# Performance work log

Hardware: AMD Instinct MI355X
Metric: run time of the kernel (lower is better)

Reference implementation:

```python
import jax, jax.numpy as jnp
import numpy as np
from jax import lax

# LiteMSA config: in_ch=256, out_ch=256, dim=8, heads=32, total_dim=256, scales=(3,)
DIM = 8
QKV_CH = 768          # 3 * total_dim
PW_GROUPS = 96        # 3 * heads


def setup_inputs() -> dict:
    key = jax.random.key(0)
    ks = jax.random.split(key, 5)
    x = jax.random.normal(ks[0], (16, 256, 64, 64), jnp.float32)
    w_qkv = jax.random.normal(ks[1], (768, 256), jnp.float32) * 0.02      # 1x1 conv
    w_dw = jax.random.normal(ks[2], (768, 1, 3, 3), jnp.float32) * 0.02   # depthwise 3x3
    w_pw = jax.random.normal(ks[3], (768, 8, 1, 1), jnp.float32) * 0.02   # grouped 1x1, 96 groups
    w_proj = jax.random.normal(ks[4], (256, 512), jnp.float32) * 0.02     # 1x1 conv
    bn_gamma = jnp.ones((256,), jnp.float32)
    bn_beta = jnp.zeros((256,), jnp.float32)
    bn_mean = jnp.zeros((256,), jnp.float32)
    bn_var = jnp.ones((256,), jnp.float32)
    return {"x": x, "w_qkv": w_qkv, "w_dw": w_dw, "w_pw": w_pw, "w_proj": w_proj,
            "bn_gamma": bn_gamma, "bn_beta": bn_beta, "bn_mean": bn_mean, "bn_var": bn_var}


def reference(x, w_qkv, w_dw, w_pw, w_proj, bn_gamma, bn_beta, bn_mean, bn_var):
    B, _, H, W = x.shape
    dn = ("NCHW", "OIHW", "NCHW")
    # qkv 1x1 conv
    qkv = jnp.einsum("bchw,oc->bohw", x, w_qkv)  # [B,768,H,W]
    # multi-scale aggregation: depthwise 3x3 -> grouped 1x1
    agg = lax.conv_general_dilated(qkv, w_dw, (1, 1), "SAME",
                                   dimension_numbers=dn, feature_group_count=QKV_CH)
    agg = lax.conv_general_dilated(agg, w_pw, (1, 1), "SAME",
                                   dimension_numbers=dn, feature_group_count=PW_GROUPS)
    ms = jnp.concatenate([qkv, agg], axis=1)  # [B,1536,H,W]
    # [B, heads_total=64, N=H*W, 3*dim]
    ms = ms.reshape(B, -1, 3 * DIM, H * W).transpose(0, 1, 3, 2)
    q = jax.nn.relu(ms[..., :DIM])
    k = jax.nn.relu(ms[..., DIM:2 * DIM])
    v = ms[..., 2 * DIM:]
    # pad v with ones for normalizer channel
    v = jnp.concatenate([v, jnp.ones(v.shape[:-1] + (1,), v.dtype)], axis=-1)  # [B,h,N,dim+1]
    kv = jnp.einsum("bhnd,bhne->bhde", k, v)   # [B,h,dim,dim+1]
    out = jnp.einsum("bhnd,bhde->bhne", q, kv)  # [B,h,N,dim+1]
    out = out[..., :DIM] / (out[..., DIM:] + 1e-15)
    out = out.transpose(0, 1, 3, 2).reshape(B, -1, H, W)  # [B,512,H,W]
    # proj 1x1 conv + BatchNorm (inference, running stats)
    y = jnp.einsum("bchw,oc->bohw", out, w_proj)
    inv = bn_gamma / jnp.sqrt(bn_var + 1e-5)
    y = y * inv[None, :, None, None] + (bn_beta - bn_mean * inv)[None, :, None, None]
    return y
```

## Files before the change

kernel.cpp:

```cpp
#include <hip/hip_runtime.h>
#include <hip/hip_bf16.h>


#define NB 16
#define CQKV 768
#define P4096 4096

typedef __bf16 bf16x8 __attribute__((ext_vector_type(8)));
typedef float f32x4 __attribute__((ext_vector_type(4)));

__device__ __forceinline__ ushort f2bf(float f) {
    union { float f; unsigned int u; } x; x.f = f;
    unsigned int u = x.u;
    unsigned int r = (u + 0x7FFFu + ((u >> 16) & 1u)) >> 16;
    return (ushort)r;
}
__device__ __forceinline__ float bf2f(ushort u) {
    union { unsigned int u; float f; } x; x.u = ((unsigned int)u) << 16;
    return x.f;
}
__device__ __forceinline__ unsigned int pk2bf(float x, float y) {
    __hip_bfloat162 h = __float22bfloat162_rn(make_float2(x, y));
    union { __hip_bfloat162 b; unsigned int u; } c; c.b = h; return c.u;
}
__device__ __forceinline__ void stage_hi8(const float* v, ushort* dh) {
    union { unsigned int u[4]; uint4 q; } H;
    #pragma unroll
    for (int i = 0; i < 4; i++) H.u[i] = pk2bf(v[2 * i], v[2 * i + 1]);
    *(uint4*)dh = H.q;
}
__device__ __forceinline__ void stage_hilo8(const float* v, ushort* dh, ushort* dl) {
    union { unsigned int u[4]; uint4 q; } H, L;
    #pragma unroll
    for (int i = 0; i < 4; i++) {
        unsigned int h = pk2bf(v[2 * i], v[2 * i + 1]);
        H.u[i] = h;
        float f0 = __uint_as_float(h << 16);
        float f1 = __uint_as_float(h & 0xffff0000u);
        L.u[i] = pk2bf(v[2 * i] - f0, v[2 * i + 1] - f1);
    }
    *(uint4*)dh = H.q;
    *(uint4*)dl = L.q;
}

__global__ __launch_bounds__(256) void gemm_qkv_q(
    const float* __restrict__ A,
    const float* __restrict__ X,
    ushort* __restrict__ Cbf,
    float*  __restrict__ qplane)
{
    const int n0 = blockIdx.x * 64;
    const int m0 = blockIdx.y * 64;
    const int b  = blockIdx.z;
    const int t  = threadIdx.x;
    const int wave = t >> 6, lane = t & 63, quad = lane >> 4, l15 = lane & 15;

    __shared__ __align__(16) ushort AsH[64][40];
    __shared__ __align__(16) ushort AsL[64][40];
    __shared__ __align__(16) ushort BsH[64][40];
    __shared__ __align__(16) ushort BsL[64][40];

    f32x4 acc[4];
    #pragma unroll
    for (int nt = 0; nt < 4; nt++)
        #pragma unroll
        for (int r = 0; r < 4; r++) acc[nt][r] = 0.0f;

    const int am = t >> 2, ak = (t & 3) * 8;
    const int arow_v = m0 + am;
    const int arow_p = (arow_v >> 3) * 24 + (arow_v & 7);
    const int bn = t & 63, kg = (t >> 6) * 8;

    for (int k0 = 0; k0 < 256; k0 += 32) {
        float av[8];
        *(float4*)&av[0] = *(const float4*)(A + (size_t)arow_p * 256 + k0 + ak);
        *(float4*)&av[4] = *(const float4*)(A + (size_t)arow_p * 256 + k0 + ak + 4);
        float bv[8];
        #pragma unroll
        for (int i = 0; i < 8; i++)
            bv[i] = X[((size_t)b * 256 + k0 + kg + i) * P4096 + n0 + bn];

        __syncthreads();
        stage_hilo8(av, &AsH[am][ak], &AsL[am][ak]);
        stage_hilo8(bv, &BsH[bn][kg], &BsL[bn][kg]);
        __syncthreads();

        bf16x8 afh = *(const bf16x8*)&AsH[wave * 16 + l15][quad * 8];
        bf16x8 afl = *(const bf16x8*)&AsL[wave * 16 + l15][quad * 8];
        #pragma unroll
        for (int nt = 0; nt < 4; nt++) {
            bf16x8 bfh = *(const bf16x8*)&BsH[nt * 16 + l15][quad * 8];
            bf16x8 bfl = *(const bf16x8*)&BsL[nt * 16 + l15][quad * 8];
            acc[nt] = __builtin_amdgcn_mfma_f32_16x16x32_bf16(afh, bfh, acc[nt], 0, 0, 0);
            acc[nt] = __builtin_amdgcn_mfma_f32_16x16x32_bf16(afl, bfh, acc[nt], 0, 0, 0);
            acc[nt] = __builtin_amdgcn_mfma_f32_16x16x32_bf16(afh, bfl, acc[nt], 0, 0, 0);
        }
    }

    #pragma unroll
    for (int nt = 0; nt < 4; nt++) {
        #pragma unroll
        for (int r = 0; r < 4; r++) {
            int rv = m0 + wave * 16 + quad * 4 + r;
            int rp = (rv >> 3) * 24 + (rv & 7);
            int col = n0 + nt * 16 + l15;
            float v = acc[nt][r];
            Cbf[((size_t)b * CQKV + rp) * P4096 + col] = f2bf(v);
            qplane[((size_t)b * 256 + rv) * P4096 + col] = v;
        }
    }
}

__global__ __launch_bounds__(256) void gemm_qkv_kv(
    const float* __restrict__ A, const float* __restrict__ X,
    ushort* __restrict__ Cbf)
{
    const int n0 = blockIdx.x * 64;
    const int m0 = blockIdx.y * 64;
    const int b  = blockIdx.z;
    const int t  = threadIdx.x;
    const int wave = t >> 6, lane = t & 63, quad = lane >> 4, l15 = lane & 15;

    __shared__ __align__(16) ushort As[64][40];
    __shared__ __align__(16) ushort Bs[64][40];

    f32x4 acc[4];
    #pragma unroll
    for (int nt = 0; nt < 4; nt++)
        #pragma unroll
        for (int r = 0; r < 4; r++) acc[nt][r] = 0.0f;

    const int am = t >> 2, ak = (t & 3) * 8;
    const int arow_v = m0 + am;
    const int arow_p = (arow_v >> 4) * 24 + 8 + (arow_v & 15);
    const int bn = t & 63, kg = (t >> 6) * 8;

    for (int k0 = 0; k0 < 256; k0 += 32) {
        float av[8];
        *(float4*)&av[0] = *(const float4*)(A + (size_t)arow_p * 256 + k0 + ak);
        *(float4*)&av[4] = *(const float4*)(A + (size_t)arow_p * 256 + k0 + ak + 4);
        float bv[8];
        #pragma unroll
        for (int i = 0; i < 8; i++)
            bv[i] = X[((size_t)b * 256 + k0 + kg + i) * P4096 + n0 + bn];

        __syncthreads();
        stage_hi8(av, &As[am][ak]);
        stage_hi8(bv, &Bs[bn][kg]);
        __syncthreads();

        bf16x8 af = *(const bf16x8*)&As[wave * 16 + l15][quad * 8];
        #pragma unroll
        for (int nt = 0; nt < 4; nt++) {
            bf16x8 bf = *(const bf16x8*)&Bs[nt * 16 + l15][quad * 8];
            acc[nt] = __builtin_amdgcn_mfma_f32_16x16x32_bf16(af, bf, acc[nt], 0, 0, 0);
        }
    }

    #pragma unroll
    for (int nt = 0; nt < 4; nt++) {
        #pragma unroll
        for (int r = 0; r < 4; r++) {
            int rv = m0 + wave * 16 + quad * 4 + r;
            int rp = (rv >> 4) * 24 + 8 + (rv & 15);
            int col = n0 + nt * 16 + l15;
            Cbf[((size_t)b * CQKV + rp) * P4096 + col] = f2bf(acc[nt][r]);
        }
    }
}

__global__ __launch_bounds__(256) void qfix_kernel(
    float* __restrict__ qplane, const float* __restrict__ w_qkv,
    const float* __restrict__ x)
{
    size_t i = (size_t)blockIdx.x * 256 + threadIdx.x;
    float q = qplane[i];
    if (fabsf(q) >= 1e-4f) return;
    int p   = (int)(i & 4095);
    int qch = (int)((i >> 12) & 255);
    int b   = (int)(i >> 20);
    int row = (qch >> 3) * 24 + (qch & 7);
    const float* wr = w_qkv + (size_t)row * 256;
    const float* xr = x + (size_t)b * 256 * P4096 + p;
    double s = 0.0;
    for (int c = 0; c < 256; c++)
        s += (double)wr[c] * (double)xr[(size_t)c * P4096];
    qplane[i] = (float)s;
}

__global__ __launch_bounds__(512, 8) void dwpw_kernel(
    const ushort* __restrict__ qkv, const float* __restrict__ wdw,
    const float* __restrict__ wpw, ushort* __restrict__ agg)
{
    const int rt = blockIdx.x;
    const int g  = blockIdx.y;
    const int b  = blockIdx.z;
    const int t  = threadIdx.x;
    const int r0 = rt * 16;
    const int cg = g * 8;

    __shared__ __align__(16) ushort tile[8][18][80];

    const ushort* src = qkv + ((size_t)(b * CQKV + cg)) * P4096;

    if (t < 288) {
        int ch = t / 36;
        int rr = (t % 36) >> 1;
        int side = t & 1;
        *(uint4*)&tile[ch][rr][side * 72] = make_uint4(0, 0, 0, 0);
    }
    #pragma unroll
    for (int i = 0; i < 3; i++) {
        int id = t + i * 512;
        if (id < 1152) {
            int ch  = id / 144;
            int rem = id - ch * 144;
            int rr  = rem >> 3;
            int oct = (rem & 7) * 8;
            int grow = r0 - 1 + rr;
            uint4 v = make_uint4(0, 0, 0, 0);
            if (grow >= 0 && grow < 64)
                v = *(const uint4*)(src + (size_t)ch * P4096 + (size_t)grow * 64 + oct);
            *(uint4*)&tile[ch][rr][8 + oct] = v;
        }
    }
    __syncthreads();

    const int kc  = t & 31;
    const int row = t >> 5;
    const float* wdwg = wdw + (size_t)cg * 9;
    const float* wpwg = wpw + (size_t)cg * 8;

    float acc0[8], acc1[8];
    #pragma unroll
    for (int oi = 0; oi < 8; oi++) { acc0[oi] = 0.0f; acc1[oi] = 0.0f; }

    #pragma unroll
    for (int c = 0; c < 8; c++) {
        float dv0 = 0.0f, dv1 = 0.0f;
        #pragma unroll
        for (int dy = 0; dy < 3; dy++) {
            const ushort* rp = &tile[c][row + dy][2 * kc + 4];
            unsigned int u1 = *(const unsigned int*)(rp + 2);
            unsigned int u2 = *(const unsigned int*)(rp + 4);
            unsigned int u3 = *(const unsigned int*)(rp + 6);
            float xm1 = __uint_as_float(u1 & 0xffff0000u);
            float x0  = __uint_as_float(u2 << 16);
            float x1  = __uint_as_float(u2 & 0xffff0000u);
            float x2  = __uint_as_float(u3 << 16);
            float w0 = wdwg[c * 9 + dy * 3 + 0];
            float w1 = wdwg[c * 9 + dy * 3 + 1];
            float w2 = wdwg[c * 9 + dy * 3 + 2];
            dv0 = fmaf(w0, xm1, dv0); dv0 = fmaf(w1, x0, dv0); dv0 = fmaf(w2, x1, dv0);
            dv1 = fmaf(w0, x0,  dv1); dv1 = fmaf(w1, x1, dv1); dv1 = fmaf(w2, x2, dv1);
        }
        #pragma unroll
        for (int oi = 0; oi < 8; oi++) {
            float w = wpwg[oi * 8 + c];
            acc0[oi] = fmaf(w, dv0, acc0[oi]);
            acc1[oi] = fmaf(w, dv1, acc1[oi]);
        }
    }

    size_t obase = ((size_t)(b * CQKV + cg)) * P4096 + (size_t)(r0 + row) * 64 + 2 * kc;
    #pragma unroll
    for (int oi = 0; oi < 8; oi++) {
        unsigned int u = (unsigned int)f2bf(acc0[oi]) |
                         ((unsigned int)f2bf(acc1[oi]) << 16);
        *(unsigned int*)&agg[obase + (size_t)oi * P4096] = u;
    }
}

__global__ __launch_bounds__(256) void kv_kernel(
    const ushort* __restrict__ qkv, const ushort* __restrict__ agg,
    float* __restrict__ kv)
{
    const int h = blockIdx.x, b = blockIdx.y, t = threadIdx.x;
    const ushort* src = (h < 32)
        ? qkv + ((size_t)(b * CQKV + h * 24)) * P4096
        : agg + ((size_t)(b * CQKV + (h - 32) * 24)) * P4096;

    float acc[72];
    #pragma unroll
    for (int i = 0; i < 72; i++) acc[i] = 0.0f;

    for (int pi = 0; pi < 16; pi++) {
        int p = t + pi * 256;
        float kvv[8], vv[8];
        #pragma unroll
        for (int d = 0; d < 8; d++) {
            float xk = bf2f(src[(size_t)(8 + d) * P4096 + p]);
            kvv[d] = xk > 0.0f ? xk : 0.0f;
        }
        #pragma unroll
        for (int e = 0; e < 8; e++) vv[e] = bf2f(src[(size_t)(16 + e) * P4096 + p]);
        #pragma unroll
        for (int d = 0; d < 8; d++) {
            #pragma unroll
            for (int e = 0; e < 8; e++) acc[d * 9 + e] += kvv[d] * vv[e];
            acc[d * 9 + 8] += kvv[d];
        }
    }

    #pragma unroll
    for (int i = 0; i < 72; i++) {
        float v = acc[i];
        #pragma unroll
        for (int off = 32; off > 0; off >>= 1) v += __shfl_xor(v, off, 64);
        acc[i] = v;
    }
    __shared__ float part[4][72];
    int wave = t >> 6, lane = t & 63;
    if (lane == 0) {
        #pragma unroll
        for (int i = 0; i < 72; i++) part[wave][i] = acc[i];
    }
    __syncthreads();
    if (t < 72)
        kv[((size_t)b * 64 + h) * 72 + t] = part[0][t] + part[1][t] + part[2][t] + part[3][t];
}

__global__ __launch_bounds__(256) void attn_out_kernel(
    const float* __restrict__ qplane, ushort* __restrict__ agg,
    const float* __restrict__ kv)
{
    const int pt = blockIdx.x, h = blockIdx.y, b = blockIdx.z, t = threadIdx.x;
    __shared__ float kvs[72];
    if (t < 72) kvs[t] = kv[((size_t)b * 64 + h) * 72 + t];
    __syncthreads();

    const bool lohead = (h < 32);
    const float* srcf = lohead
        ? qplane + ((size_t)(b * 256 + h * 8)) * P4096 : nullptr;
    const ushort* srcb = lohead ? nullptr
        : agg + ((size_t)(b * CQKV + (h - 32) * 24)) * P4096;

    int p = pt * 256 + t;
    float num[8]; float den = 0.0f;
    #pragma unroll
    for (int e = 0; e < 8; e++) num[e] = 0.0f;
    #pragma unroll
    for (int d = 0; d < 8; d++) {
        float q = lohead ? srcf[(size_t)d * P4096 + p]
                         : bf2f(srcb[(size_t)d * P4096 + p]);
        q = q > 0.0f ? q : 0.0f;
        #pragma unroll
        for (int e = 0; e < 8; e++) num[e] += q * kvs[d * 9 + e];
        den += q * kvs[d * 9 + 8];
    }
    float rd = 1.0f / (den + 1e-15f);
    ushort* dst = agg + ((size_t)(b * CQKV + (h / 2) * 24 + 8 + (h % 2) * 8)) * P4096 + p;
    #pragma unroll
    for (int e = 0; e < 8; e++)
        dst[(size_t)e * P4096] = f2bf(num[e] * rd);
}

__global__ __launch_bounds__(256) void gemm_proj(
    const float* __restrict__ A,
    const ushort* __restrict__ Bagg,
    float* __restrict__ Y,
    const float* __restrict__ bn_g, const float* __restrict__ bn_b,
    const float* __restrict__ bn_m, const float* __restrict__ bn_v)
{
    const int n0 = blockIdx.x * 64;
    const int m0 = blockIdx.y * 64;
    const int b  = blockIdx.z;
    const int t  = threadIdx.x;
    const int wave = t >> 6, lane = t & 63, quad = lane >> 4, l15 = lane & 15;

    __shared__ __align__(16) ushort As[64][40];
    __shared__ __align__(16) ushort Bs[64][40];

    f32x4 acc[4];
    #pragma unroll
    for (int nt = 0; nt < 4; nt++)
        #pragma unroll
        for (int r = 0; r < 4; r++) acc[nt][r] = 0.0f;

    const int am = t >> 2, ak = (t & 3) * 8;
    const int bn = t & 63, kg = (t >> 6) * 8;

    for (int k0 = 0; k0 < 512; k0 += 32) {
        float av[8];
        *(float4*)&av[0] = *(const float4*)(A + (size_t)(m0 + am) * 512 + k0 + ak);
        *(float4*)&av[4] = *(const float4*)(A + (size_t)(m0 + am) * 512 + k0 + ak + 4);
        ushort bu[8];
        #pragma unroll
        for (int i = 0; i < 8; i++) {
            int kk = k0 + kg + i;
            int amch = (kk >> 4) * 24 + 8 + (kk & 15);
            bu[i] = Bagg[((size_t)b * CQKV + amch) * P4096 + n0 + bn];
        }

        __syncthreads();
        stage_hi8(av, &As[am][ak]);
        {
            union { ushort us[8]; uint4 q; } Bp;
            #pragma unroll
            for (int i = 0; i < 8; i++) Bp.us[i] = bu[i];
            *(uint4*)&Bs[bn][kg] = Bp.q;
        }
        __syncthreads();

        bf16x8 af = *(const bf16x8*)&As[wave * 16 + l15][quad * 8];
        #pragma unroll
        for (int nt = 0; nt < 4; nt++) {
            bf16x8 bf = *(const bf16x8*)&Bs[nt * 16 + l15][quad * 8];
            acc[nt] = __builtin_amdgcn_mfma_f32_16x16x32_bf16(af, bf, acc[nt], 0, 0, 0);
        }
    }

    #pragma unroll
    for (int nt = 0; nt < 4; nt++) {
        #pragma unroll
        for (int r = 0; r < 4; r++) {
            int row = m0 + wave * 16 + quad * 4 + r;
            int col = n0 + nt * 16 + l15;
            float inv = bn_g[row] / sqrtf(bn_v[row] + 1e-5f);
            float v = acc[nt][r] * inv + (bn_b[row] - bn_m[row] * inv);
            Y[((size_t)b * 256 + row) * P4096 + col] = v;
        }
    }
}

extern "C" void kernel_launch(void* const* d_in, const int* in_sizes, int n_in,
                              void* d_out, int out_size, void* d_ws, size_t ws_size,
                              hipStream_t stream) {
    const float* x      = (const float*)d_in[0];
    const float* w_qkv  = (const float*)d_in[1];
    const float* w_dw   = (const float*)d_in[2];
    const float* w_pw   = (const float*)d_in[3];
    const float* w_proj = (const float*)d_in[4];
    const float* bn_g   = (const float*)d_in[5];
    const float* bn_b   = (const float*)d_in[6];
    const float* bn_m   = (const float*)d_in[7];
    const float* bn_v   = (const float*)d_in[8];
    float* y = (float*)d_out;

    char* ws = (char*)d_ws;
    ushort* qkv_bf = (ushort*)(ws);
    float*  qplane = (float*) (ws + 100663296);
    ushort* agg_bf = (ushort*)(ws + 167772160);
    float*  kvbuf  = (float*)d_out;

    gemm_qkv_q<<<dim3(64, 4, NB), 256, 0, stream>>>(w_qkv, x, qkv_bf, qplane);
    gemm_qkv_kv<<<dim3(64, 8, NB), 256, 0, stream>>>(w_qkv, x, qkv_bf);

    qfix_kernel<<<65536, 256, 0, stream>>>(qplane, w_qkv, x);

    dwpw_kernel<<<dim3(4, 96, NB), 512, 0, stream>>>(qkv_bf, w_dw, w_pw, agg_bf);

    kv_kernel<<<dim3(64, NB), 256, 0, stream>>>(qkv_bf, agg_bf, kvbuf);

    attn_out_kernel<<<dim3(16, 64, NB), 256, 0, stream>>>(qplane, agg_bf, kvbuf);

    gemm_proj<<<dim3(64, 4, NB), 256, 0, stream>>>(
        w_proj, agg_bf, y, bn_g, bn_b, bn_m, bn_v);
}
```

Measured before the change: 457.1 us.

## Pre-convert inputs to swizzled bf16 and fuse QKV GEMMs with LDS direct loads

```diff
diff --git a/kernel.cpp b/kernel.cpp
--- a/kernel.cpp
+++ b/kernel.cpp
@@ -8,6 +8,8 @@
 
 typedef __bf16 bf16x8 __attribute__((ext_vector_type(8)));
 typedef float f32x4 __attribute__((ext_vector_type(4)));
+
+#define MFMA_BF16 __builtin_amdgcn_mfma_f32_16x16x32_bf16
 
 __device__ __forceinline__ ushort f2bf(float f) {
     union { float f; unsigned int u; } x; x.f = f;
@@ -29,143 +31,204 @@
     for (int i = 0; i < 4; i++) H.u[i] = pk2bf(v[2 * i], v[2 * i + 1]);
     *(uint4*)dh = H.q;
 }
-__device__ __forceinline__ void stage_hilo8(const float* v, ushort* dh, ushort* dl) {
-    union { unsigned int u[4]; uint4 q; } H, L;
-    #pragma unroll
-    for (int i = 0; i < 4; i++) {
-        unsigned int h = pk2bf(v[2 * i], v[2 * i + 1]);
-        H.u[i] = h;
-        float f0 = __uint_as_float(h << 16);
-        float f1 = __uint_as_float(h & 0xffff0000u);
-        L.u[i] = pk2bf(v[2 * i] - f0, v[2 * i + 1] - f1);
-    }
-    *(uint4*)dh = H.q;
-    *(uint4*)dl = L.q;
-}
-
-__global__ __launch_bounds__(256) void gemm_qkv_q(
-    const float* __restrict__ A,
-    const float* __restrict__ X,
-    ushort* __restrict__ Cbf,
-    float*  __restrict__ qplane)
-{
-    const int n0 = blockIdx.x * 64;
-    const int m0 = blockIdx.y * 64;
+
+__device__ __forceinline__ void gload16(void* lds, const void* g) {
+    __builtin_amdgcn_global_load_lds(
+        (const __attribute__((address_space(1))) void*)g,
+        (__attribute__((address_space(3))) void*)lds, 16, 0, 0);
+}
+
+__global__ __launch_bounds__(128) void conv_w(
+    const float* __restrict__ W, ushort* __restrict__ Ah, ushort* __restrict__ Al)
+{
+    const int rv = blockIdx.x;
+    const int t  = threadIdx.x;
+    int phys;
+    if (rv < 256) phys = (rv >> 3) * 24 + (rv & 7);
+    else { int r2 = rv - 256; phys = (r2 >> 4) * 24 + 8 + (r2 & 15); }
+    int c = t * 2;
+    float w0 = W[(size_t)phys * 256 + c];
+    float w1 = W[(size_t)phys * 256 + c + 1];
+    unsigned int h = pk2bf(w0, w1);
+    float f0 = __uint_as_float(h << 16);
+    float f1 = __uint_as_float(h & 0xffff0000u);
+    unsigned int l = pk2bf(w0 - f0, w1 - f1);
+    int sl = ((c >> 3) & 3) ^ ((rv >> 1) & 3);
+    int idx = (c & ~31) + sl * 8 + (c & 7);
+    *(unsigned int*)&Ah[(size_t)rv * 256 + idx] = h;
+    *(unsigned int*)&Al[(size_t)rv * 256 + idx] = l;
+}
+
+__global__ __launch_bounds__(256) void conv_x(
+    const float* __restrict__ X, ushort* __restrict__ XTh, ushort* __restrict__ XTl)
+{
+    const int pt = blockIdx.x;
+    const int ct = blockIdx.y;
+    const int b  = blockIdx.z;
+    const int t  = threadIdx.x;
+    const int p0 = pt * 64, c0 = ct * 64;
+
+    __shared__ float tile[64][65];
+
+    {
+        int cr = t >> 2, pc = (t & 3) * 16;
+        const float* xr = X + ((size_t)b * 256 + c0 + cr) * P4096 + p0 + pc;
+        float4 v0 = *(const float4*)xr;
+        float4 v1 = *(const float4*)(xr + 4);
+        float4 v2 = *(const float4*)(xr + 8);
+        float4 v3 = *(const float4*)(xr + 12);
+        float* d = &tile[cr][pc];
+        d[0]=v0.x; d[1]=v0.y; d[2]=v0.z; d[3]=v0.w;
+        d[4]=v1.x; d[5]=v1.y; d[6]=v1.z; d[7]=v1.w;
+        d[8]=v2.x; d[9]=v2.y; d[10]=v2.z; d[11]=v2.w;
+        d[12]=v3.x; d[13]=v3.y; d[14]=v3.z; d[15]=v3.w;
+    }
+    __syncthreads();
+
+    #pragma unroll
+    for (int pass = 0; pass < 2; pass++) {
+        int tp = t >> 2;
+        int cc = (t & 3) + pass * 4;
+        int p  = p0 + tp;
+        float v[8];
+        #pragma unroll
+        for (int j = 0; j < 8; j++) v[j] = tile[cc * 8 + j][tp];
+        union { unsigned int u[4]; uint4 q; } H, L;
+        #pragma unroll
+        for (int i = 0; i < 4; i++) {
+            unsigned int h = pk2bf(v[2 * i], v[2 * i + 1]);
+            H.u[i] = h;
+            float f0 = __uint_as_float(h << 16);
+            float f1 = __uint_as_float(h & 0xffff0000u);
+            L.u[i] = pk2bf(v[2 * i] - f0, v[2 * i + 1] - f1);
+        }
+        int c = c0 + cc * 8;
+        int sl = ((c >> 3) & 3) ^ ((p >> 1) & 3);
+        size_t idx = ((size_t)b * P4096 + p) * 256 + (c & ~31) + sl * 8;
+        *(uint4*)&XTh[idx] = H.q;
+        *(uint4*)&XTl[idx] = L.q;
+    }
+}
+
+__global__ __launch_bounds__(256, 3) void gemm_fused(
+    const ushort* __restrict__ Ah, const ushort* __restrict__ Al,
+    const ushort* __restrict__ Bh, const ushort* __restrict__ Bl,
+    ushort* __restrict__ Cbf, float* __restrict__ qplane)
+{
+    const int mt = blockIdx.x;
+    const int n0 = blockIdx.y * 128;
     const int b  = blockIdx.z;
     const int t  = threadIdx.x;
     const int wave = t >> 6, lane = t & 63, quad = lane >> 4, l15 = lane & 15;
-
-    __shared__ __align__(16) ushort AsH[64][40];
-    __shared__ __align__(16) ushort AsL[64][40];
-    __shared__ __align__(16) ushort BsH[64][40];
-    __shared__ __align__(16) ushort BsL[64][40];
-
-    f32x4 acc[4];
-    #pragma unroll
-    for (int nt = 0; nt < 4; nt++)
-        #pragma unroll
-        for (int r = 0; r < 4; r++) acc[nt][r] = 0.0f;
-
-    const int am = t >> 2, ak = (t & 3) * 8;
-    const int arow_v = m0 + am;
-    const int arow_p = (arow_v >> 3) * 24 + (arow_v & 7);
-    const int bn = t & 63, kg = (t >> 6) * 8;
-
-    for (int k0 = 0; k0 < 256; k0 += 32) {
-        float av[8];
-        *(float4*)&av[0] = *(const float4*)(A + (size_t)arow_p * 256 + k0 + ak);
-        *(float4*)&av[4] = *(const float4*)(A + (size_t)arow_p * 256 + k0 + ak + 4);
-        float bv[8];
-        #pragma unroll
-        for (int i = 0; i < 8; i++)
-            bv[i] = X[((size_t)b * 256 + k0 + kg + i) * P4096 + n0 + bn];
-
-        __syncthreads();
-        stage_hilo8(av, &AsH[am][ak], &AsL[am][ak]);
-        stage_hilo8(bv, &BsH[bn][kg], &BsL[bn][kg]);
-        __syncthreads();
-
-        bf16x8 afh = *(const bf16x8*)&AsH[wave * 16 + l15][quad * 8];
-        bf16x8 afl = *(const bf16x8*)&AsL[wave * 16 + l15][quad * 8];
-        #pragma unroll
-        for (int nt = 0; nt < 4; nt++) {
-            bf16x8 bfh = *(const bf16x8*)&BsH[nt * 16 + l15][quad * 8];
-            bf16x8 bfl = *(const bf16x8*)&BsL[nt * 16 + l15][quad * 8];
-            acc[nt] = __builtin_amdgcn_mfma_f32_16x16x32_bf16(afh, bfh, acc[nt], 0, 0, 0);
-            acc[nt] = __builtin_amdgcn_mfma_f32_16x16x32_bf16(afl, bfh, acc[nt], 0, 0, 0);
-            acc[nt] = __builtin_amdgcn_mfma_f32_16x16x32_bf16(afh, bfl, acc[nt], 0, 0, 0);
-        }
-    }
-
-    #pragma unroll
-    for (int nt = 0; nt < 4; nt++) {
-        #pragma unroll
-        for (int r = 0; r < 4; r++) {
-            int rv = m0 + wave * 16 + quad * 4 + r;
-            int rp = (rv >> 3) * 24 + (rv & 7);
-            int col = n0 + nt * 16 + l15;
-            float v = acc[nt][r];
-            Cbf[((size_t)b * CQKV + rp) * P4096 + col] = f2bf(v);
-            qplane[((size_t)b * 256 + rv) * P4096 + col] = v;
-        }
-    }
-}
-
-__global__ __launch_bounds__(256) void gemm_qkv_kv(
-    const float* __restrict__ A, const float* __restrict__ X,
-    ushort* __restrict__ Cbf)
-{
-    const int n0 = blockIdx.x * 64;
-    const int m0 = blockIdx.y * 64;
-    const int b  = blockIdx.z;
-    const int t  = threadIdx.x;
-    const int wave = t >> 6, lane = t & 63, quad = lane >> 4, l15 = lane & 15;
-
-    __shared__ __align__(16) ushort As[64][40];
-    __shared__ __align__(16) ushort Bs[64][40];
-
-    f32x4 acc[4];
-    #pragma unroll
-    for (int nt = 0; nt < 4; nt++)
-        #pragma unroll
-        for (int r = 0; r < 4; r++) acc[nt][r] = 0.0f;
-
-    const int am = t >> 2, ak = (t & 3) * 8;
-    const int arow_v = m0 + am;
-    const int arow_p = (arow_v >> 4) * 24 + 8 + (arow_v & 15);
-    const int bn = t & 63, kg = (t >> 6) * 8;
-
-    for (int k0 = 0; k0 < 256; k0 += 32) {
-        float av[8];
-        *(float4*)&av[0] = *(const float4*)(A + (size_t)arow_p * 256 + k0 + ak);
-        *(float4*)&av[4] = *(const float4*)(A + (size_t)arow_p * 256 + k0 + ak + 4);
-        float bv[8];
-        #pragma unroll
-        for (int i = 0; i < 8; i++)
-            bv[i] = X[((size_t)b * 256 + k0 + kg + i) * P4096 + n0 + bn];
-
-        __syncthreads();
-        stage_hi8(av, &As[am][ak]);
-        stage_hi8(bv, &Bs[bn][kg]);
-        __syncthreads();
-
-        bf16x8 af = *(const bf16x8*)&As[wave * 16 + l15][quad * 8];
-        #pragma unroll
-        for (int nt = 0; nt < 4; nt++) {
-            bf16x8 bf = *(const bf16x8*)&Bs[nt * 16 + l15][quad * 8];
-            acc[nt] = __builtin_amdgcn_mfma_f32_16x16x32_bf16(af, bf, acc[nt], 0, 0, 0);
-        }
-    }
-
-    #pragma unroll
-    for (int nt = 0; nt < 4; nt++) {
-        #pragma unroll
-        for (int r = 0; r < 4; r++) {
-            int rv = m0 + wave * 16 + quad * 4 + r;
-            int rp = (rv >> 4) * 24 + 8 + (rv & 15);
-            int col = n0 + nt * 16 + l15;
-            Cbf[((size_t)b * CQKV + rp) * P4096 + col] = f2bf(acc[nt][r]);
-        }
+    const int wr = wave >> 1, wc = wave & 1;
+    const int M0 = mt * 128;
+
+    __shared__ __align__(16) ushort AsH[128 * 32];
+    __shared__ __align__(16) ushort AsL[128 * 32];
+    __shared__ __align__(16) ushort BsH[128 * 32];
+    __shared__ __align__(16) ushort BsL[128 * 32];
+
+    int aoff[4], boff[4];
+    #pragma unroll
+    for (int i = 0; i < 4; i++) {
+        int ra = wr * 64 + i * 16 + l15;
+        aoff[i] = ra * 64 + ((quad ^ ((ra >> 1) & 3)) << 4);
+        int rb = wc * 64 + i * 16 + l15;
+        boff[i] = rb * 64 + ((quad ^ ((rb >> 1) & 3)) << 4);
+    }
+
+    const int srow = t >> 2;
+    const int schunk = (t & 3) * 8;
+    const size_t abase = (size_t)(M0 + srow) * 256 + schunk;
+    const size_t bbase = ((size_t)b * P4096 + n0 + srow) * 256 + schunk;
+    const int ldsoff = wave * 1024;
+
+    f32x4 acc[4][4];
+    #pragma unroll
+    for (int mi = 0; mi < 4; mi++)
+        #pragma unroll
+        for (int nj = 0; nj < 4; nj++)
+            #pragma unroll
+            for (int r = 0; r < 4; r++) acc[mi][nj][r] = 0.0f;
+
+    if (mt < 2) {
+        for (int kw = 0; kw < 8; kw++) {
+            __syncthreads();
+            #pragma unroll
+            for (int i = 0; i < 2; i++) {
+                int lo = ldsoff + i * 4096;
+                size_t so = (size_t)(i * 64) * 256 + kw * 32;
+                gload16((char*)AsH + lo, Ah + abase + so);
+                gload16((char*)AsL + lo, Al + abase + so);
+                gload16((char*)BsH + lo, Bh + bbase + so);
+                gload16((char*)BsL + lo, Bl + bbase + so);
+            }
+            __syncthreads();
+            bf16x8 ah[4], al[4];
+            #pragma unroll
+            for (int mi = 0; mi < 4; mi++) {
+                ah[mi] = *(const bf16x8*)((const char*)AsH + aoff[mi]);
+                al[mi] = *(const bf16x8*)((const char*)AsL + aoff[mi]);
+            }
+            #pragma unroll
+            for (int nj = 0; nj < 4; nj++) {
+                bf16x8 bh = *(const bf16x8*)((const char*)BsH + boff[nj]);
+                bf16x8 bl = *(const bf16x8*)((const char*)BsL + boff[nj]);
+                #pragma unroll
+                for (int mi = 0; mi < 4; mi++) {
+                    acc[mi][nj] = MFMA_BF16(ah[mi], bh, acc[mi][nj], 0, 0, 0);
+                    acc[mi][nj] = MFMA_BF16(al[mi], bh, acc[mi][nj], 0, 0, 0);
+                    acc[mi][nj] = MFMA_BF16(ah[mi], bl, acc[mi][nj], 0, 0, 0);
+                }
+            }
+        }
+        #pragma unroll
+        for (int mi = 0; mi < 4; mi++)
+            #pragma unroll
+            for (int nj = 0; nj < 4; nj++)
+                #pragma unroll
+                for (int r = 0; r < 4; r++) {
+                    int rv = M0 + wr * 64 + mi * 16 + quad * 4 + r;
+                    int rp = (rv >> 3) * 24 + (rv & 7);
+                    int col = n0 + wc * 64 + nj * 16 + l15;
+                    float v = acc[mi][nj][r];
+                    Cbf[((size_t)b * CQKV + rp) * P4096 + col] = f2bf(v);
+                    qplane[((size_t)b * 256 + rv) * P4096 + col] = v;
+                }
+    } else {
+        for (int kw = 0; kw < 8; kw++) {
+            __syncthreads();
+            #pragma unroll
+            for (int i = 0; i < 2; i++) {
+                int lo = ldsoff + i * 4096;
+                size_t so = (size_t)(i * 64) * 256 + kw * 32;
+                gload16((char*)AsH + lo, Ah + abase + so);
+                gload16((char*)BsH + lo, Bh + bbase + so);
+            }
+            __syncthreads();
+            bf16x8 ah[4];
+            #pragma unroll
+            for (int mi = 0; mi < 4; mi++)
+                ah[mi] = *(const bf16x8*)((const char*)AsH + aoff[mi]);
+            #pragma unroll
+            for (int nj = 0; nj < 4; nj++) {
+                bf16x8 bh = *(const bf16x8*)((const char*)BsH + boff[nj]);
+                #pragma unroll
+                for (int mi = 0; mi < 4; mi++)
+                    acc[mi][nj] = MFMA_BF16(ah[mi], bh, acc[mi][nj], 0, 0, 0);
+            }
+        }
+        #pragma unroll
+        for (int mi = 0; mi < 4; mi++)
+            #pragma unroll
+            for (int nj = 0; nj < 4; nj++)
+                #pragma unroll
+                for (int r = 0; r < 4; r++) {
+                    int rv2 = (M0 - 256) + wr * 64 + mi * 16 + quad * 4 + r;
+                    int rp = (rv2 >> 4) * 24 + 8 + (rv2 & 15);
+                    int col = n0 + wc * 64 + nj * 16 + l15;
+                    Cbf[((size_t)b * CQKV + rp) * P4096 + col] = f2bf(acc[mi][nj][r]);
+                }
     }
 }
 
@@ -406,7 +469,7 @@
         #pragma unroll
         for (int nt = 0; nt < 4; nt++) {
             bf16x8 bf = *(const bf16x8*)&Bs[nt * 16 + l15][quad * 8];
-            acc[nt] = __builtin_amdgcn_mfma_f32_16x16x32_bf16(af, bf, acc[nt], 0, 0, 0);
+            acc[nt] = MFMA_BF16(af, bf, acc[nt], 0, 0, 0);
         }
     }
 
@@ -441,10 +504,17 @@
     ushort* qkv_bf = (ushort*)(ws);
     float*  qplane = (float*) (ws + 100663296);
     ushort* agg_bf = (ushort*)(ws + 167772160);
+    ushort* XTh = (ushort*)(ws + 167772160);
+    ushort* XTl = (ushort*)(ws + 167772160 + 33554432);
+    ushort* Awh = (ushort*)(ws + 167772160 + 67108864);
+    ushort* Awl = (ushort*)(ws + 167772160 + 67108864 + 393216);
     float*  kvbuf  = (float*)d_out;
 
-    gemm_qkv_q<<<dim3(64, 4, NB), 256, 0, stream>>>(w_qkv, x, qkv_bf, qplane);
-    gemm_qkv_kv<<<dim3(64, 8, NB), 256, 0, stream>>>(w_qkv, x, qkv_bf);
+    conv_w<<<dim3(768), 128, 0, stream>>>(w_qkv, Awh, Awl);
+    conv_x<<<dim3(64, 4, NB), 256, 0, stream>>>(x, XTh, XTl);
+
+    gemm_fused<<<dim3(6, 32, NB), 256, 0, stream>>>(
+        Awh, Awl, XTh, XTl, qkv_bf, qplane);
 
     qfix_kernel<<<65536, 256, 0, stream>>>(qplane, w_qkv, x);
 
```

Result: no change. 451.3 us (-1.3%).
